# Performance work log

Hardware: AMD Instinct MI355X
Metric: run time of the kernel (lower is better)

Reference implementation:

```python
import jax, jax.numpy as jnp
import numpy as np

B, S = 128, 512
VOCAB, E, H, T = 100000, 100, 128, 10  # tagset_size=10 -> CRF over T-1=9 tags
HD = H // 2  # per-direction LSTM hidden


def setup_inputs():
    key = jax.random.key(0)
    ks = jax.random.split(key, 14)
    s = 0.08
    inputs = jax.random.randint(ks[0], (B, S), 1, VOCAB)
    tags = jax.random.randint(ks[1], (B, S), 1, T)  # valid after tags-1 shift
    mask = jnp.ones((B, S), dtype=bool)
    emb = (jax.random.normal(ks[2], (VOCAB, E)) * s).at[0].set(0.0)  # padding_idx=0 row zeroed
    Wih_f = jax.random.normal(ks[3], (4 * HD, E)) * s
    Whh_f = jax.random.normal(ks[4], (4 * HD, HD)) * s
    b_f = jax.random.normal(ks[5], (4 * HD,)) * s
    Wih_b = jax.random.normal(ks[6], (4 * HD, E)) * s
    Whh_b = jax.random.normal(ks[7], (4 * HD, HD)) * s
    b_b = jax.random.normal(ks[8], (4 * HD,)) * s
    W_out = jax.random.normal(ks[9], (T, H)) * s
    b_out = jax.random.normal(ks[10], (T,)) * s
    start = jax.random.normal(ks[11], (T - 1,)) * s
    end = jax.random.normal(ks[12], (T - 1,)) * s
    trans = jax.random.normal(ks[13], (T - 1, T - 1)) * s
    return dict(inputs=inputs, tags=tags, mask=mask, emb=emb,
                Wih_f=Wih_f, Whh_f=Whh_f, b_f=b_f,
                Wih_b=Wih_b, Whh_b=Whh_b, b_b=b_b,
                W_out=W_out, b_out=b_out, start=start, end=end, trans=trans)


def _lstm_dir(x, Wih, Whh, b, reverse):
    # x: [S, B, E] time-major; PyTorch gate order i,f,g,o; b = b_ih + b_hh
    h0 = jnp.zeros((x.shape[1], Whh.shape[1]), x.dtype)

    def step(carry, xt):
        h, c = carry
        gates = xt @ Wih.T + h @ Whh.T + b
        i, f, g, o = jnp.split(gates, 4, axis=-1)
        c = jax.nn.sigmoid(f) * c + jax.nn.sigmoid(i) * jnp.tanh(g)
        h = jax.nn.sigmoid(o) * jnp.tanh(c)
        return (h, c), h

    _, hs = jax.lax.scan(step, (h0, h0), x, reverse=reverse)
    return hs  # [S, B, HD]


def _crf_nll(em, tags, mask, start, end, trans):
    # Linear-chain CRF (torchcrf-style). em: [S,B,K], tags/mask: [S,B]
    pick = lambda e, t: jnp.take_along_axis(e, t[:, None], axis=-1)[:, 0]
    # numerator: score of the gold path
    score0 = start[tags[0]] + pick(em[0], tags[0])

    def num_step(sc, inp):
        em_t, t, tp, m = inp
        return sc + jnp.where(m, trans[tp, t] + pick(em_t, t), 0.0), None

    score, _ = jax.lax.scan(num_step, score0, (em[1:], tags[1:], tags[:-1], mask[1:]))
    last_idx = mask.sum(0).astype(jnp.int32) - 1
    last_tags = jnp.take_along_axis(tags, last_idx[None, :], axis=0)[0]
    score = score + end[last_tags]
    # denominator: forward algorithm (log partition)
    alpha0 = start[None, :] + em[0]  # [B,K]

    def fwd_step(alpha, inp):
        em_t, m = inp
        nxt = jax.nn.logsumexp(alpha[:, :, None] + trans[None, :, :] + em_t[:, None, :], axis=1)
        return jnp.where(m[:, None], nxt, alpha), None

    alpha, _ = jax.lax.scan(fwd_step, alpha0, (em[1:], mask[1:]))
    logZ = jax.nn.logsumexp(alpha + end[None, :], axis=1)
    return -(score - logZ).mean()  # loss = -log_likelihood.mean()


def _forward(inputs, tags, mask, emb, Wih_f, Whh_f, b_f, Wih_b, Whh_b, b_b, W_out, b_out, start, end, trans):
    x = emb[inputs].transpose(1, 0, 2)  # [S,B,E]
    h = jnp.concatenate([_lstm_dir(x, Wih_f, Whh_f, b_f, False),
                         _lstm_dir(x, Wih_b, Whh_b, b_b, True)], axis=-1)  # [S,B,H]
    # dropout is identity at eval; slice off tag 0 as in the module
    em = (h @ W_out.T + b_out)[:, :, 1:]  # [S,B,T-1]
    return _crf_nll(em, (tags - 1).T, mask.T, start, end, trans)


def reference(inputs, tags, mask, emb, Wih_f, Whh_f, b_f, Wih_b, Whh_b, b_b, W_out, b_out, start, end, trans):
    return _forward(inputs, tags, mask, emb, Wih_f, Whh_f, b_f, Wih_b, Whh_b, b_b, W_out, b_out, start, end, trans)
```

## Files before the change

kernel.cpp:

```cpp
#include <hip/hip_runtime.h>
#include <math.h>

#define SB 512
#define NB 128
#define HD 64

typedef _Float16 h2 __attribute__((ext_vector_type(2)));
union U4 { uint4 u; h2 h[4]; _Float16 f[8]; };
union U2 { uint2 u; _Float16 f[4]; };
union UH { unsigned u; _Float16 f[2]; };

__device__ __forceinline__ float frcp(float x) { return __builtin_amdgcn_rcpf(x); }
__device__ __forceinline__ float fsig(float x) { return frcp(1.0f + __expf(-x)); }
__device__ __forceinline__ float ftanh(float x) {
    float t = __expf(-2.0f * fabsf(x));
    float r = (1.0f - t) * frcp(1.0f + t);
    return copysignf(r, x);
}
__device__ __forceinline__ float fdot2(h2 a, h2 b, float c) {
    return __builtin_amdgcn_fdot2(a, b, c, false);
}

__global__ void prep_kernel(const float* __restrict__ Wih_f, const float* __restrict__ Wih_bb,
                            const float* __restrict__ Whh_f, const float* __restrict__ Whh_bb,
                            const float* __restrict__ b_f, const float* __restrict__ b_bb,
                            const float* __restrict__ trans,
                            unsigned* __restrict__ W2h, unsigned* __restrict__ whh16,
                            float* __restrict__ bias2, float* __restrict__ Eexp)
{
    int idx = blockIdx.x * 256 + threadIdx.x;
    if (idx < 26624) {
        int col = idx / 52, d = idx - col * 52;
        int dir = col >> 8, r = col & 255, j = r >> 2, g = r & 3;
        const float* src = (dir ? Wih_bb : Wih_f) + (g * 64 + j) * 100;
        UH u; u.u = 0;
        if (d < 50) { u.f[0] = (_Float16)src[2 * d]; u.f[1] = (_Float16)src[2 * d + 1]; }
        W2h[idx] = u.u;
    } else if (idx < 43008) {
        int d = idx - 26624;
        int kp = d & 31, u = (d >> 5) & 63, g = (d >> 11) & 3, dir = d >> 13;
        const float* src = (dir ? Whh_bb : Whh_f) + (g * 64 + u) * 64 + 2 * kp;
        UH uu; uu.f[0] = (_Float16)src[0]; uu.f[1] = (_Float16)src[1];
        whh16[d] = uu.u;
    } else if (idx < 43520) {
        int col = idx - 43008;
        int dir = col >> 8, r = col & 255, j = r >> 2, g = r & 3;
        bias2[col] = (dir ? b_bb : b_f)[g * 64 + j];
    } else if (idx < 43601) {
        int i = idx - 43520;
        Eexp[i] = __expf(trans[i]);
    }
}

__global__ __launch_bounds__(256, 1) void gemm_kernel(
    const int* __restrict__ inputs, const float* __restrict__ emb,
    const unsigned* __restrict__ W2h, const float* __restrict__ bias2,
    _Float16* __restrict__ xgh)
{
    __shared__ __align__(16) unsigned sE[128 * 52];
    __shared__ __align__(16) unsigned sW[128 * 52];
    __shared__ int stok[128];
    const int tt = blockIdx.x;
    const int tid = threadIdx.x;

    if (tid < 128) stok[tid] = inputs[tid * SB + tt];
    __syncthreads();
    for (int idx = tid; idx < 6656; idx += 256) {
        int row = idx / 52, d = idx - row * 52;
        int token = stok[row];
        UH u; u.u = 0;
        if (d < 50) {
            const float* ep = emb + (size_t)token * 100 + 2 * d;
            u.f[0] = (_Float16)ep[0]; u.f[1] = (_Float16)ep[1];
        }
        sE[idx] = u.u;
    }

    const int tx = tid & 15, ty = tid >> 4;

    for (int cb4 = 0; cb4 < 4; ++cb4) {
        const int cb = cb4 * 128;
        __syncthreads();
        for (int idx = tid; idx < 1664; idx += 256)
            ((uint4*)sW)[idx] = ((const uint4*)W2h)[cb * 13 + idx];
        __syncthreads();

        float acc[8][8];
        #pragma unroll
        for (int r = 0; r < 8; ++r)
            #pragma unroll
            for (int i = 0; i < 8; ++i) acc[r][i] = 0.f;

        for (int kk = 0; kk < 13; ++kk) {
            U4 e[8], wv[8];
            #pragma unroll
            for (int r = 0; r < 8; ++r) e[r].u = ((const uint4*)sE)[(ty + 16 * r) * 13 + kk];
            #pragma unroll
            for (int i = 0; i < 8; ++i) wv[i].u = ((const uint4*)sW)[(tx + 16 * i) * 13 + kk];
            #pragma unroll
            for (int r = 0; r < 8; ++r)
                #pragma unroll
                for (int i = 0; i < 8; ++i) {
                    float a = acc[r][i];
                    #pragma unroll
                    for (int q = 0; q < 4; ++q) a = fdot2(e[r].h[q], wv[i].h[q], a);
                    acc[r][i] = a;
                }
        }

        #pragma unroll
        for (int i = 0; i < 8; ++i) {
            int col = cb + tx + 16 * i;
            float bc = bias2[col];
            #pragma unroll
            for (int r = 0; r < 8; ++r) {
                int row = tt * NB + ty + 16 * r;
                xgh[(size_t)row * 512 + col] = (_Float16)(acc[r][i] + bc);
            }
        }
    }
}

__global__ __attribute__((amdgpu_flat_work_group_size(64, 64), amdgpu_waves_per_eu(1, 1)))
void lstm_kernel(
    const _Float16* __restrict__ xgh, const unsigned* __restrict__ whh16,
    _Float16* __restrict__ h16)
{
    const int blk = blockIdx.x;
    const int b = blk & (NB - 1);
    const int dir = blk >> 7;
    const int j = threadIdx.x;

    U4 w[32];
    const uint4* W4 = (const uint4*)(whh16 + dir * 8192);
    #pragma unroll
    for (int g = 0; g < 4; ++g)
        #pragma unroll
        for (int k4 = 0; k4 < 8; ++k4)
            w[g * 8 + k4].u = W4[(g * 64 + j) * 8 + k4];
    #pragma unroll
    for (int i = 0; i < 32; ++i)
        asm volatile("" : "+v"(w[i].u.x), "+v"(w[i].u.y), "+v"(w[i].u.z), "+v"(w[i].u.w));

    __shared__ __align__(16) _Float16 hbuf[64];
    hbuf[j] = (_Float16)0.f;
    float c = 0.f;

    const int t0 = dir ? (SB - 1) : 0;
    const ptrdiff_t xstride = (dir ? -1 : 1) * (ptrdiff_t)(NB * 512);
    const _Float16* xp = xgh + ((size_t)(t0 * NB + b)) * 512 + dir * 256 + j * 4;
    _Float16* hp = h16 + ((size_t)(b * 2 + dir) * SB + t0) * 64 + j;
    const ptrdiff_t hstride = (dir ? -1 : 1) * (ptrdiff_t)64;

    U2 p0, p1, p2;
    p0.u = *(const uint2*)xp;
    p1.u = *(const uint2*)(xp + xstride);
    p2.u = *(const uint2*)(xp + 2 * xstride);
    const _Float16* xq = xp + 3 * xstride;

    for (int s = 0; s < SB; ++s) {
        float a0 = (float)p0.f[0], a1 = (float)p0.f[1];
        float a2 = (float)p0.f[2], a3 = (float)p0.f[3];
        p0 = p1; p1 = p2;
        p2.u = *(const uint2*)xq;
        xq += xstride;

        U4 hv[8];
        #pragma unroll
        for (int k4 = 0; k4 < 8; ++k4) hv[k4].u = *(const uint4*)&hbuf[k4 * 8];

        float g0[4] = {a0, 0.f, 0.f, 0.f};
        float g1[4] = {a1, 0.f, 0.f, 0.f};
        float g2[4] = {a2, 0.f, 0.f, 0.f};
        float g3[4] = {a3, 0.f, 0.f, 0.f};
        #pragma unroll
        for (int k4 = 0; k4 < 8; ++k4) {
            const int p = k4 & 3;
            #pragma unroll
            for (int q = 0; q < 4; ++q) {
                g0[p] = fdot2(hv[k4].h[q], w[0 * 8 + k4].h[q], g0[p]);
                g1[p] = fdot2(hv[k4].h[q], w[1 * 8 + k4].h[q], g1[p]);
                g2[p] = fdot2(hv[k4].h[q], w[2 * 8 + k4].h[q], g2[p]);
                g3[p] = fdot2(hv[k4].h[q], w[3 * 8 + k4].h[q], g3[p]);
            }
        }
        a0 = (g0[0] + g0[1]) + (g0[2] + g0[3]);
        a1 = (g1[0] + g1[1]) + (g1[2] + g1[3]);
        a2 = (g2[0] + g2[1]) + (g2[2] + g2[3]);
        a3 = (g3[0] + g3[1]) + (g3[2] + g3[3]);

        float ig = fsig(a0), fg = fsig(a1), gg = ftanh(a2), og = fsig(a3);
        c = fg * c + ig * gg;
        float h = og * ftanh(c);
        *hp = (_Float16)h;
        hp += hstride;
        hbuf[j] = (_Float16)h;
    }
}

__global__ __launch_bounds__(256, 1) void proj_kernel(
    const _Float16* __restrict__ h16, const float* __restrict__ W_out,
    const float* __restrict__ b_out, float* __restrict__ em3)
{
    __shared__ __align__(16) unsigned tile[128 * 64];
    __shared__ __align__(16) unsigned sWo[9 * 64];
    __shared__ float sb[9];
    const int b = blockIdx.x, tid = threadIdx.x;

    for (int i2 = tid; i2 < 576; i2 += 256) {
        int k = i2 >> 6, jp = i2 & 63;
        const float* src = W_out + (k + 1) * 128 + 2 * jp;
        UH u; u.f[0] = (_Float16)src[0]; u.f[1] = (_Float16)src[1];
        sWo[i2] = u.u;
    }
    if (tid < 9) sb[tid] = b_out[1 + tid];

    float* dst0 = em3 + (size_t)b * (SB * 12);

    for (int tt = 0; tt < 4; ++tt) {
        const int t0 = tt * 128;
        __syncthreads();
        #pragma unroll
        for (int dir = 0; dir < 2; ++dir) {
            const unsigned* src = (const unsigned*)(h16 + ((size_t)(b * 2 + dir) * SB + t0) * 64);
            for (int i = tid; i < 4096; i += 256) {
                int t = i >> 5, jp = i & 31;
                tile[t * 64 + dir * 32 + jp] = src[i];
            }
        }
        __syncthreads();

        for (int o = tid; o < 1152; o += 256) {
            int tl = o / 9, k = o - 9 * tl;
            const U4* hr = (const U4*)&tile[tl * 64];
            const U4* wr = (const U4*)&sWo[k * 64];
            float pa = 0.f, pb = 0.f;
            #pragma unroll
            for (int q = 0; q < 16; q += 2) {
                U4 hv = hr[q], wv = wr[q];
                U4 hv2 = hr[q + 1], wv2 = wr[q + 1];
                #pragma unroll
                for (int z = 0; z < 4; ++z) {
                    pa = fdot2(hv.h[z], wv.h[z], pa);
                    pb = fdot2(hv2.h[z], wv2.h[z], pb);
                }
            }
            dst0[(t0 + tl) * 12 + k] = pa + pb + sb[k];
        }
    }
}

__global__ __launch_bounds__(64, 1) void crf_gold(
    const float* __restrict__ em3, const int* __restrict__ tags,
    const float* __restrict__ startv, const float* __restrict__ endv,
    const float* __restrict__ trans, float* __restrict__ gold)
{
    const int b = blockIdx.x, l = threadIdx.x;
    const int* tb = tags + (size_t)b * SB;
    const float* eb = em3 + (size_t)b * (SB * 12);
    float sc = 0.f;
    for (int t = l; t < SB; t += 64) {
        int tg = tb[t] - 1;
        if (t > 0) {
            int tp = tb[t - 1] - 1;
            sc += trans[tp * 9 + tg] + eb[t * 12 + tg];
        }
    }
    if (l == 0) {
        int tg0 = tb[0] - 1, tgl = tb[SB - 1] - 1;
        sc += startv[tg0] + eb[tg0] + endv[tgl];
    }
    #pragma unroll
    for (int off = 32; off > 0; off >>= 1) sc += __shfl_down(sc, off);
    if (l == 0) gold[b] = sc;
}

__global__ __launch_bounds__(256, 1) void crf_scan(
    const float* __restrict__ em3, const float* __restrict__ Eexp,
    float* __restrict__ Pws)
{
    const int lane = blockIdx.x * 256 + threadIdx.x;
    const int c = lane & 31, b = lane >> 5;

    float E[81];
    #pragma unroll
    for (int i = 0; i < 81; ++i) E[i] = Eexp[i];

    float P[81];
    #pragma unroll
    for (int i = 0; i < 81; ++i) P[i] = 0.f;
    #pragma unroll
    for (int i = 0; i < 9; ++i) P[i * 9 + i] = 1.f;
    float M = 0.f;

    const int t0 = 1 + 16 * c;
    const int nst = (t0 + 16 <= SB) ? 16 : (SB - t0);
    const float* ep = em3 + (size_t)b * (SB * 12) + t0 * 12;

    for (int s = 0; s < nst; ++s, ep += 12) {
        float4 e0 = *(const float4*)ep;
        float4 e1 = *(const float4*)(ep + 4);
        float e8 = ep[8];
        float ex[9] = { __expf(e0.x), __expf(e0.y), __expf(e0.z), __expf(e0.w),
                        __expf(e1.x), __expf(e1.y), __expf(e1.z), __expf(e1.w),
                        __expf(e8) };
        #pragma unroll
        for (int i = 0; i < 9; ++i) {
            float tmp[9];
            #pragma unroll
            for (int jj = 0; jj < 9; ++jj) tmp[jj] = P[i * 9] * E[jj];
            #pragma unroll
            for (int k = 1; k < 9; ++k)
                #pragma unroll
                for (int jj = 0; jj < 9; ++jj) tmp[jj] += P[i * 9 + k] * E[k * 9 + jj];
            #pragma unroll
            for (int jj = 0; jj < 9; ++jj) P[i * 9 + jj] = tmp[jj] * ex[jj];
        }
        if ((s & 3) == 3) {
            float mx = P[0];
            #pragma unroll
            for (int i = 1; i < 81; ++i) mx = fmaxf(mx, P[i]);
            M += __logf(mx);
            float r = frcp(mx);
            #pragma unroll
            for (int i = 0; i < 81; ++i) P[i] *= r;
        }
    }

    float* dst = Pws + (size_t)lane * 84;
    #pragma unroll
    for (int i = 0; i < 81; ++i) dst[i] = P[i];
    dst[81] = M;
}

__global__ __launch_bounds__(128, 1) void crf_combine(
    const float* __restrict__ em3, const float* __restrict__ Pws,
    const float* __restrict__ gold, const float* __restrict__ startv,
    const float* __restrict__ endv, float* __restrict__ out)
{
    const int b = threadIdx.x;
    float A[9], M = 0.f;
    {
        const float* eb = em3 + (size_t)b * (SB * 12);
        float4 e0 = *(const float4*)eb;
        float4 e1 = *(const float4*)(eb + 4);
        float e[9] = { e0.x, e0.y, e0.z, e0.w, e1.x, e1.y, e1.z, e1.w, eb[8] };
        #pragma unroll
        for (int k = 0; k < 9; ++k) A[k] = __expf(startv[k] + e[k]);
    }

    for (int c = 0; c < 32; ++c) {
        const float4* src = (const float4*)(Pws + ((size_t)b * 32 + c) * 84);
        float buf[84];
        #pragma unroll
        for (int q = 0; q < 21; ++q) {
            float4 v = src[q];
            buf[4 * q] = v.x; buf[4 * q + 1] = v.y; buf[4 * q + 2] = v.z; buf[4 * q + 3] = v.w;
        }
        float tmp[9];
        #pragma unroll
        for (int jj = 0; jj < 9; ++jj) tmp[jj] = A[0] * buf[jj];
        #pragma unroll
        for (int i = 1; i < 9; ++i)
            #pragma unroll
            for (int jj = 0; jj < 9; ++jj) tmp[jj] += A[i] * buf[i * 9 + jj];
        float mx = tmp[0];
        #pragma unroll
        for (int jj = 1; jj < 9; ++jj) mx = fmaxf(mx, tmp[jj]);
        M += __logf(mx) + buf[81];
        float r = frcp(mx);
        #pragma unroll
        for (int jj = 0; jj < 9; ++jj) A[jj] = tmp[jj] * r;
    }

    float Z = 0.f;
    #pragma unroll
    for (int k = 0; k < 9; ++k) Z += A[k] * __expf(endv[k]);
    float part = M + __logf(Z) - gold[b];

    #pragma unroll
    for (int off = 32; off > 0; off >>= 1) part += __shfl_down(part, off);
    __shared__ float sm[2];
    if ((b & 63) == 0) sm[b >> 6] = part;
    __syncthreads();
    if (b == 0) out[0] = (sm[0] + sm[1]) * (1.0f / NB);
}

extern "C" void kernel_launch(void* const* d_in, const int* in_sizes, int n_in,
                              void* d_out, int out_size, void* d_ws, size_t ws_size,
                              hipStream_t stream)
{
    const int*   inputs = (const int*)d_in[0];
    const int*   tags   = (const int*)d_in[1];
    const float* emb    = (const float*)d_in[3];
    const float* Wih_f  = (const float*)d_in[4];
    const float* Whh_f  = (const float*)d_in[5];
    const float* b_f    = (const float*)d_in[6];
    const float* Wih_b  = (const float*)d_in[7];
    const float* Whh_b  = (const float*)d_in[8];
    const float* b_b    = (const float*)d_in[9];
    const float* W_out  = (const float*)d_in[10];
    const float* b_out  = (const float*)d_in[11];
    const float* startv = (const float*)d_in[12];
    const float* endv   = (const float*)d_in[13];
    const float* transv = (const float*)d_in[14];

    char* w = (char*)d_ws;
    float* em3     = (float*)w;     w += (size_t)NB * SB * 12 * 4;
    _Float16* xgh  = (_Float16*)w;  w += (size_t)SB * NB * 512 * 2;
    _Float16* h16  = (_Float16*)w;  w += (size_t)NB * 2 * SB * 64 * 2;
    float* Pws     = (float*)w;     w += (size_t)NB * 32 * 84 * 4;
    float* gold    = (float*)w;     w += NB * 4;
    unsigned* W2h  = (unsigned*)w;  w += 26624 * 4;
    unsigned* whh16= (unsigned*)w;  w += 16384 * 4;
    float* bias2   = (float*)w;     w += 512 * 4;
    float* Eexp    = (float*)w;     w += 81 * 4;

    prep_kernel<<<171, 256, 0, stream>>>(Wih_f, Wih_b, Whh_f, Whh_b, b_f, b_b, transv,
                                         W2h, whh16, bias2, Eexp);
    gemm_kernel<<<SB, 256, 0, stream>>>(inputs, emb, W2h, bias2, xgh);
    lstm_kernel<<<256, 64, 0, stream>>>(xgh, whh16, h16);
    proj_kernel<<<NB, 256, 0, stream>>>(h16, W_out, b_out, em3);
    crf_gold<<<NB, 64, 0, stream>>>(em3, tags, startv, endv, transv, gold);
    crf_scan<<<16, 256, 0, stream>>>(em3, Eexp, Pws);
    crf_combine<<<1, 128, 0, stream>>>(em3, Pws, gold, startv, endv, (float*)d_out);
}
```

Before: 549.6 us.

## Split LSTM hidden-unit dot products across two lanes with double-buffered h

The LSTM recurrence kernel now runs 128 threads per sequence/direction, with each hidden unit's 64-wide dot product split across a lane pair and combined via a shuffle. Each thread keeps half the recurrent weights in registers. The shared hidden-state buffer is double-buffered and a block barrier is added each step, since two waves now cooperate. This halves the serial per-step FMA chain on the latency-bound recurrence, at the cost of a __syncthreads per timestep and a cross-lane shuffle.

```diff
diff --git a/kernel.cpp b/kernel.cpp
--- a/kernel.cpp
+++ b/kernel.cpp
@@ -121,7 +121,7 @@
     }
 }
 
-__global__ __attribute__((amdgpu_flat_work_group_size(64, 64), amdgpu_waves_per_eu(1, 1)))
+__global__ __attribute__((amdgpu_flat_work_group_size(128, 128), amdgpu_waves_per_eu(1, 1)))
 void lstm_kernel(
     const _Float16* __restrict__ xgh, const unsigned* __restrict__ whh16,
     _Float16* __restrict__ h16)
@@ -129,27 +129,27 @@
     const int blk = blockIdx.x;
     const int b = blk & (NB - 1);
     const int dir = blk >> 7;
-    const int j = threadIdx.x;
-
-    U4 w[32];
-    const uint4* W4 = (const uint4*)(whh16 + dir * 8192);
+    const int tid = threadIdx.x;
+    const int wv = tid >> 6, l = tid & 63;
+    const int u = wv * 32 + (l >> 1);
+    const int kh = l & 1;
+
+    U4 w[4][4];
+    const uint4* W4 = (const uint4*)whh16;
     #pragma unroll
     for (int g = 0; g < 4; ++g)
         #pragma unroll
-        for (int k4 = 0; k4 < 8; ++k4)
-            w[g * 8 + k4].u = W4[(g * 64 + j) * 8 + k4];
-    #pragma unroll
-    for (int i = 0; i < 32; ++i)
-        asm volatile("" : "+v"(w[i].u.x), "+v"(w[i].u.y), "+v"(w[i].u.z), "+v"(w[i].u.w));
-
-    __shared__ __align__(16) _Float16 hbuf[64];
-    hbuf[j] = (_Float16)0.f;
+        for (int q = 0; q < 4; ++q)
+            w[g][q].u = W4[((dir * 4 + g) * 64 + u) * 8 + kh * 4 + q];
+
+    __shared__ __align__(16) _Float16 hbuf[2][64];
+    if (tid < 64) hbuf[0][tid] = (_Float16)0.f;
     float c = 0.f;
 
     const int t0 = dir ? (SB - 1) : 0;
     const ptrdiff_t xstride = (dir ? -1 : 1) * (ptrdiff_t)(NB * 512);
-    const _Float16* xp = xgh + ((size_t)(t0 * NB + b)) * 512 + dir * 256 + j * 4;
-    _Float16* hp = h16 + ((size_t)(b * 2 + dir) * SB + t0) * 64 + j;
+    const _Float16* xp = xgh + ((size_t)(t0 * NB + b)) * 512 + dir * 256 + u * 4;
+    _Float16* hp = h16 + ((size_t)(b * 2 + dir) * SB + t0) * 64 + u;
     const ptrdiff_t hstride = (dir ? -1 : 1) * (ptrdiff_t)64;
 
     U2 p0, p1, p2;
@@ -157,44 +157,45 @@
     p1.u = *(const uint2*)(xp + xstride);
     p2.u = *(const uint2*)(xp + 2 * xstride);
     const _Float16* xq = xp + 3 * xstride;
+    __syncthreads();
 
     for (int s = 0; s < SB; ++s) {
-        float a0 = (float)p0.f[0], a1 = (float)p0.f[1];
-        float a2 = (float)p0.f[2], a3 = (float)p0.f[3];
+        const int par = s & 1;
+        U4 hv[4];
+        #pragma unroll
+        for (int q = 0; q < 4; ++q)
+            hv[q].u = *(const uint4*)&hbuf[par][kh * 32 + q * 8];
+
+        float pa[4], pb[4];
+        #pragma unroll
+        for (int g = 0; g < 4; ++g) { pa[g] = 0.f; pb[g] = 0.f; }
+        #pragma unroll
+        for (int q = 0; q < 4; ++q)
+            #pragma unroll
+            for (int g = 0; g < 4; ++g) {
+                pa[g] = fdot2(hv[q].h[0], w[g][q].h[0], pa[g]);
+                pa[g] = fdot2(hv[q].h[1], w[g][q].h[1], pa[g]);
+                pb[g] = fdot2(hv[q].h[2], w[g][q].h[2], pb[g]);
+                pb[g] = fdot2(hv[q].h[3], w[g][q].h[3], pb[g]);
+            }
+
+        float a[4];
+        #pragma unroll
+        for (int g = 0; g < 4; ++g) {
+            float sg = pa[g] + pb[g];
+            a[g] = sg + __shfl_xor(sg, 1, 64) + (float)p0.f[g];
+        }
         p0 = p1; p1 = p2;
         p2.u = *(const uint2*)xq;
         xq += xstride;
 
-        U4 hv[8];
-        #pragma unroll
-        for (int k4 = 0; k4 < 8; ++k4) hv[k4].u = *(const uint4*)&hbuf[k4 * 8];
-
-        float g0[4] = {a0, 0.f, 0.f, 0.f};
-        float g1[4] = {a1, 0.f, 0.f, 0.f};
-        float g2[4] = {a2, 0.f, 0.f, 0.f};
-        float g3[4] = {a3, 0.f, 0.f, 0.f};
-        #pragma unroll
-        for (int k4 = 0; k4 < 8; ++k4) {
-            const int p = k4 & 3;
-            #pragma unroll
-            for (int q = 0; q < 4; ++q) {
-                g0[p] = fdot2(hv[k4].h[q], w[0 * 8 + k4].h[q], g0[p]);
-                g1[p] = fdot2(hv[k4].h[q], w[1 * 8 + k4].h[q], g1[p]);
-                g2[p] = fdot2(hv[k4].h[q], w[2 * 8 + k4].h[q], g2[p]);
-                g3[p] = fdot2(hv[k4].h[q], w[3 * 8 + k4].h[q], g3[p]);
-            }
-        }
-        a0 = (g0[0] + g0[1]) + (g0[2] + g0[3]);
-        a1 = (g1[0] + g1[1]) + (g1[2] + g1[3]);
-        a2 = (g2[0] + g2[1]) + (g2[2] + g2[3]);
-        a3 = (g3[0] + g3[1]) + (g3[2] + g3[3]);
-
-        float ig = fsig(a0), fg = fsig(a1), gg = ftanh(a2), og = fsig(a3);
+        float ig = fsig(a[0]), fg = fsig(a[1]), gg = ftanh(a[2]), og = fsig(a[3]);
         c = fg * c + ig * gg;
         float h = og * ftanh(c);
-        *hp = (_Float16)h;
+        hbuf[par ^ 1][u] = (_Float16)h;
+        if (kh == 0) *hp = (_Float16)h;
         hp += hstride;
-        hbuf[j] = (_Float16)h;
+        __syncthreads();
     }
 }
 
@@ -419,7 +420,7 @@
     prep_kernel<<<171, 256, 0, stream>>>(Wih_f, Wih_b, Whh_f, Whh_b, b_f, b_b, transv,
                                          W2h, whh16, bias2, Eexp);
     gemm_kernel<<<SB, 256, 0, stream>>>(inputs, emb, W2h, bias2, xgh);
-    lstm_kernel<<<256, 64, 0, stream>>>(xgh, whh16, h16);
+    lstm_kernel<<<256, 128, 0, stream>>>(xgh, whh16, h16);
     proj_kernel<<<NB, 256, 0, stream>>>(h16, W_out, b_out, em3);
     crf_gold<<<NB, 64, 0, stream>>>(em3, tags, startv, endv, transv, gold);
     crf_scan<<<16, 256, 0, stream>>>(em3, Eexp, Pws);
```

After: 556.6 us. About the same (+1.3%).

## Fuse projection and CRF stages into one per-sequence kernel using shared memory

Applied to the files above, without the earlier changes.

Merges the output projection, gold-path score, chunked CRF forward scan and chunk combine into a single kernel per batch row. Emissions and chunk transfer matrices stay in shared memory, and the final loss is accumulated with an atomic add into an output zeroed by a memset. This removes three launches and the global round trips for emissions and partial matrices. In exchange the CRF scan now uses only 32 threads per block on 128 blocks, and the LSTM weight register pinning is removed while a barrier is added before its loop.

```diff
diff --git a/kernel.cpp b/kernel.cpp
--- a/kernel.cpp
+++ b/kernel.cpp
@@ -24,9 +24,8 @@
 __global__ void prep_kernel(const float* __restrict__ Wih_f, const float* __restrict__ Wih_bb,
                             const float* __restrict__ Whh_f, const float* __restrict__ Whh_bb,
                             const float* __restrict__ b_f, const float* __restrict__ b_bb,
-                            const float* __restrict__ trans,
                             unsigned* __restrict__ W2h, unsigned* __restrict__ whh16,
-                            float* __restrict__ bias2, float* __restrict__ Eexp)
+                            float* __restrict__ bias2)
 {
     int idx = blockIdx.x * 256 + threadIdx.x;
     if (idx < 26624) {
@@ -46,9 +45,6 @@
         int col = idx - 43008;
         int dir = col >> 8, r = col & 255, j = r >> 2, g = r & 3;
         bias2[col] = (dir ? b_bb : b_f)[g * 64 + j];
-    } else if (idx < 43601) {
-        int i = idx - 43520;
-        Eexp[i] = __expf(trans[i]);
     }
 }
 
@@ -138,9 +134,6 @@
         #pragma unroll
         for (int k4 = 0; k4 < 8; ++k4)
             w[g * 8 + k4].u = W4[(g * 64 + j) * 8 + k4];
-    #pragma unroll
-    for (int i = 0; i < 32; ++i)
-        asm volatile("" : "+v"(w[i].u.x), "+v"(w[i].u.y), "+v"(w[i].u.z), "+v"(w[i].u.w));
 
     __shared__ __align__(16) _Float16 hbuf[64];
     hbuf[j] = (_Float16)0.f;
@@ -157,6 +150,7 @@
     p1.u = *(const uint2*)(xp + xstride);
     p2.u = *(const uint2*)(xp + 2 * xstride);
     const _Float16* xq = xp + 3 * xstride;
+    __syncthreads();
 
     for (int s = 0; s < SB; ++s) {
         float a0 = (float)p0.f[0], a1 = (float)p0.f[1];
@@ -198,14 +192,21 @@
     }
 }
 
-__global__ __launch_bounds__(256, 1) void proj_kernel(
+__global__ __launch_bounds__(256, 1) void fused_crf(
     const _Float16* __restrict__ h16, const float* __restrict__ W_out,
-    const float* __restrict__ b_out, float* __restrict__ em3)
-{
+    const float* __restrict__ b_out, const int* __restrict__ tags,
+    const float* __restrict__ startv, const float* __restrict__ endv,
+    const float* __restrict__ trans, float* __restrict__ out)
+{
+    __shared__ __align__(16) float emc[16 * 32 * 9];
+    __shared__ __align__(16) float em0[12];
     __shared__ __align__(16) unsigned tile[128 * 64];
     __shared__ __align__(16) unsigned sWo[9 * 64];
     __shared__ float sb[9];
+    __shared__ float sgold;
+
     const int b = blockIdx.x, tid = threadIdx.x;
+    float* chout = (float*)tile;
 
     for (int i2 = tid; i2 < 576; i2 += 256) {
         int k = i2 >> 6, jp = i2 & 63;
@@ -215,8 +216,6 @@
     }
     if (tid < 9) sb[tid] = b_out[1 + tid];
 
-    float* dst0 = em3 + (size_t)b * (SB * 12);
-
     for (int tt = 0; tt < 4; ++tt) {
         const int t0 = tt * 128;
         __syncthreads();
@@ -245,145 +244,117 @@
                     pb = fdot2(hv2.h[z], wv2.h[z], pb);
                 }
             }
-            dst0[(t0 + tl) * 12 + k] = pa + pb + sb[k];
-        }
-    }
-}
-
-__global__ __launch_bounds__(64, 1) void crf_gold(
-    const float* __restrict__ em3, const int* __restrict__ tags,
-    const float* __restrict__ startv, const float* __restrict__ endv,
-    const float* __restrict__ trans, float* __restrict__ gold)
-{
-    const int b = blockIdx.x, l = threadIdx.x;
-    const int* tb = tags + (size_t)b * SB;
-    const float* eb = em3 + (size_t)b * (SB * 12);
-    float sc = 0.f;
-    for (int t = l; t < SB; t += 64) {
-        int tg = tb[t] - 1;
-        if (t > 0) {
-            int tp = tb[t - 1] - 1;
-            sc += trans[tp * 9 + tg] + eb[t * 12 + tg];
-        }
-    }
-    if (l == 0) {
-        int tg0 = tb[0] - 1, tgl = tb[SB - 1] - 1;
-        sc += startv[tg0] + eb[tg0] + endv[tgl];
-    }
-    #pragma unroll
-    for (int off = 32; off > 0; off >>= 1) sc += __shfl_down(sc, off);
-    if (l == 0) gold[b] = sc;
-}
-
-__global__ __launch_bounds__(256, 1) void crf_scan(
-    const float* __restrict__ em3, const float* __restrict__ Eexp,
-    float* __restrict__ Pws)
-{
-    const int lane = blockIdx.x * 256 + threadIdx.x;
-    const int c = lane & 31, b = lane >> 5;
-
-    float E[81];
-    #pragma unroll
-    for (int i = 0; i < 81; ++i) E[i] = Eexp[i];
-
-    float P[81];
-    #pragma unroll
-    for (int i = 0; i < 81; ++i) P[i] = 0.f;
-    #pragma unroll
-    for (int i = 0; i < 9; ++i) P[i * 9 + i] = 1.f;
-    float M = 0.f;
-
-    const int t0 = 1 + 16 * c;
-    const int nst = (t0 + 16 <= SB) ? 16 : (SB - t0);
-    const float* ep = em3 + (size_t)b * (SB * 12) + t0 * 12;
-
-    for (int s = 0; s < nst; ++s, ep += 12) {
-        float4 e0 = *(const float4*)ep;
-        float4 e1 = *(const float4*)(ep + 4);
-        float e8 = ep[8];
-        float ex[9] = { __expf(e0.x), __expf(e0.y), __expf(e0.z), __expf(e0.w),
-                        __expf(e1.x), __expf(e1.y), __expf(e1.z), __expf(e1.w),
-                        __expf(e8) };
-        #pragma unroll
-        for (int i = 0; i < 9; ++i) {
+            float v = pa + pb + sb[k];
+            int t = t0 + tl;
+            if (t == 0) em0[k] = v;
+            else        emc[(((t - 1) & 15) * 32 + ((t - 1) >> 4)) * 9 + k] = v;
+        }
+    }
+    __syncthreads();
+
+    if (tid >= 64 && tid < 128) {
+        const int l = tid - 64;
+        const int* tb = tags + (size_t)b * SB;
+        float sc = 0.f;
+        for (int t = l; t < SB; t += 64) {
+            int tg = tb[t] - 1;
+            if (t > 0) {
+                int tp = tb[t - 1] - 1;
+                sc += trans[tp * 9 + tg] + emc[(((t - 1) & 15) * 32 + ((t - 1) >> 4)) * 9 + tg];
+            }
+        }
+        if (l == 0) {
+            int tg0 = tb[0] - 1, tgl = tb[SB - 1] - 1;
+            sc += startv[tg0] + em0[tg0] + endv[tgl];
+        }
+        #pragma unroll
+        for (int off = 32; off > 0; off >>= 1) sc += __shfl_down(sc, off);
+        if (l == 0) sgold = sc;
+    }
+
+    if (tid < 32) {
+        const int c = tid;
+        float E[81];
+        #pragma unroll
+        for (int i = 0; i < 81; ++i) E[i] = __expf(trans[i]);
+
+        float P[81];
+        #pragma unroll
+        for (int i = 0; i < 81; ++i) P[i] = 0.f;
+        #pragma unroll
+        for (int i = 0; i < 9; ++i) P[i * 9 + i] = 1.f;
+        float M = 0.f;
+
+        const int t0c = 1 + 16 * c;
+        const int nst = (t0c + 16 <= SB) ? 16 : (SB - t0c);
+        for (int s = 0; s < nst; ++s) {
+            const float* ep = &emc[(s * 32 + c) * 9];
+            float ex[9];
+            #pragma unroll
+            for (int k = 0; k < 9; ++k) ex[k] = __expf(ep[k]);
+            #pragma unroll
+            for (int i = 0; i < 9; ++i) {
+                float tmp[9];
+                #pragma unroll
+                for (int jj = 0; jj < 9; ++jj) tmp[jj] = P[i * 9] * E[jj];
+                #pragma unroll
+                for (int k = 1; k < 9; ++k)
+                    #pragma unroll
+                    for (int jj = 0; jj < 9; ++jj) tmp[jj] += P[i * 9 + k] * E[k * 9 + jj];
+                #pragma unroll
+                for (int jj = 0; jj < 9; ++jj) P[i * 9 + jj] = tmp[jj] * ex[jj];
+            }
+            if ((s & 3) == 3) {
+                float mx = P[0];
+                #pragma unroll
+                for (int i = 1; i < 81; ++i) mx = fmaxf(mx, P[i]);
+                M += __logf(mx);
+                float r = frcp(mx);
+                #pragma unroll
+                for (int i = 0; i < 81; ++i) P[i] *= r;
+            }
+        }
+        float* dst = &chout[c * 84];
+        #pragma unroll
+        for (int i = 0; i < 81; ++i) dst[i] = P[i];
+        dst[81] = M;
+    }
+    __syncthreads();
+
+    if (tid == 0) {
+        float A[9], M = 0.f;
+        #pragma unroll
+        for (int k = 0; k < 9; ++k) A[k] = __expf(startv[k] + em0[k]);
+
+        for (int c = 0; c < 32; ++c) {
+            const float4* src = (const float4*)&chout[c * 84];
+            float buf[84];
+            #pragma unroll
+            for (int q = 0; q < 21; ++q) {
+                float4 v = src[q];
+                buf[4 * q] = v.x; buf[4 * q + 1] = v.y; buf[4 * q + 2] = v.z; buf[4 * q + 3] = v.w;
+            }
             float tmp[9];
             #pragma unroll
-            for (int jj = 0; jj < 9; ++jj) tmp[jj] = P[i * 9] * E[jj];
-            #pragma unroll
-            for (int k = 1; k < 9; ++k)
-                #pragma unroll
-                for (int jj = 0; jj < 9; ++jj) tmp[jj] += P[i * 9 + k] * E[k * 9 + jj];
-            #pragma unroll
-            for (int jj = 0; jj < 9; ++jj) P[i * 9 + jj] = tmp[jj] * ex[jj];
-        }
-        if ((s & 3) == 3) {
-            float mx = P[0];
-            #pragma unroll
-            for (int i = 1; i < 81; ++i) mx = fmaxf(mx, P[i]);
-            M += __logf(mx);
+            for (int jj = 0; jj < 9; ++jj) tmp[jj] = A[0] * buf[jj];
+            #pragma unroll
+            for (int i = 1; i < 9; ++i)
+                #pragma unroll
+                for (int jj = 0; jj < 9; ++jj) tmp[jj] += A[i] * buf[i * 9 + jj];
+            float mx = tmp[0];
+            #pragma unroll
+            for (int jj = 1; jj < 9; ++jj) mx = fmaxf(mx, tmp[jj]);
+            M += __logf(mx) + buf[81];
             float r = frcp(mx);
             #pragma unroll
-            for (int i = 0; i < 81; ++i) P[i] *= r;
-        }
-    }
-
-    float* dst = Pws + (size_t)lane * 84;
-    #pragma unroll
-    for (int i = 0; i < 81; ++i) dst[i] = P[i];
-    dst[81] = M;
-}
-
-__global__ __launch_bounds__(128, 1) void crf_combine(
-    const float* __restrict__ em3, const float* __restrict__ Pws,
-    const float* __restrict__ gold, const float* __restrict__ startv,
-    const float* __restrict__ endv, float* __restrict__ out)
-{
-    const int b = threadIdx.x;
-    float A[9], M = 0.f;
-    {
-        const float* eb = em3 + (size_t)b * (SB * 12);
-        float4 e0 = *(const float4*)eb;
-        float4 e1 = *(const float4*)(eb + 4);
-        float e[9] = { e0.x, e0.y, e0.z, e0.w, e1.x, e1.y, e1.z, e1.w, eb[8] };
-        #pragma unroll
-        for (int k = 0; k < 9; ++k) A[k] = __expf(startv[k] + e[k]);
-    }
-
-    for (int c = 0; c < 32; ++c) {
-        const float4* src = (const float4*)(Pws + ((size_t)b * 32 + c) * 84);
-        float buf[84];
-        #pragma unroll
-        for (int q = 0; q < 21; ++q) {
-            float4 v = src[q];
-            buf[4 * q] = v.x; buf[4 * q + 1] = v.y; buf[4 * q + 2] = v.z; buf[4 * q + 3] = v.w;
-        }
-        float tmp[9];
-        #pragma unroll
-        for (int jj = 0; jj < 9; ++jj) tmp[jj] = A[0] * buf[jj];
-        #pragma unroll
-        for (int i = 1; i < 9; ++i)
-            #pragma unroll
-            for (int jj = 0; jj < 9; ++jj) tmp[jj] += A[i] * buf[i * 9 + jj];
-        float mx = tmp[0];
-        #pragma unroll
-        for (int jj = 1; jj < 9; ++jj) mx = fmaxf(mx, tmp[jj]);
-        M += __logf(mx) + buf[81];
-        float r = frcp(mx);
-        #pragma unroll
-        for (int jj = 0; jj < 9; ++jj) A[jj] = tmp[jj] * r;
-    }
-
-    float Z = 0.f;
-    #pragma unroll
-    for (int k = 0; k < 9; ++k) Z += A[k] * __expf(endv[k]);
-    float part = M + __logf(Z) - gold[b];
-
-    #pragma unroll
-    for (int off = 32; off > 0; off >>= 1) part += __shfl_down(part, off);
-    __shared__ float sm[2];
-    if ((b & 63) == 0) sm[b >> 6] = part;
-    __syncthreads();
-    if (b == 0) out[0] = (sm[0] + sm[1]) * (1.0f / NB);
+            for (int jj = 0; jj < 9; ++jj) A[jj] = tmp[jj] * r;
+        }
+        float Z = 0.f;
+        #pragma unroll
+        for (int k = 0; k < 9; ++k) Z += A[k] * __expf(endv[k]);
+        float part = M + __logf(Z) - sgold;
+        atomicAdd(out, part * (1.0f / NB));
+    }
 }
 
 extern "C" void kernel_launch(void* const* d_in, const int* in_sizes, int n_in,
@@ -406,22 +377,18 @@
     const float* transv = (const float*)d_in[14];
 
     char* w = (char*)d_ws;
-    float* em3     = (float*)w;     w += (size_t)NB * SB * 12 * 4;
+    w += 4 * 1024 * 1024;
     _Float16* xgh  = (_Float16*)w;  w += (size_t)SB * NB * 512 * 2;
     _Float16* h16  = (_Float16*)w;  w += (size_t)NB * 2 * SB * 64 * 2;
-    float* Pws     = (float*)w;     w += (size_t)NB * 32 * 84 * 4;
-    float* gold    = (float*)w;     w += NB * 4;
     unsigned* W2h  = (unsigned*)w;  w += 26624 * 4;
     unsigned* whh16= (unsigned*)w;  w += 16384 * 4;
     float* bias2   = (float*)w;     w += 512 * 4;
-    float* Eexp    = (float*)w;     w += 81 * 4;
-
-    prep_kernel<<<171, 256, 0, stream>>>(Wih_f, Wih_b, Whh_f, Whh_b, b_f, b_b, transv,
-                                         W2h, whh16, bias2, Eexp);
+
+    hipMemsetAsync(d_out, 0, sizeof(float), stream);
+    prep_kernel<<<171, 256, 0, stream>>>(Wih_f, Wih_b, Whh_f, Whh_b, b_f, b_b,
+                                         W2h, whh16, bias2);
     gemm_kernel<<<SB, 256, 0, stream>>>(inputs, emb, W2h, bias2, xgh);
     lstm_kernel<<<256, 64, 0, stream>>>(xgh, whh16, h16);
-    proj_kernel<<<NB, 256, 0, stream>>>(h16, W_out, b_out, em3);
-    crf_gold<<<NB, 64, 0, stream>>>(em3, tags, startv, endv, transv, gold);
-    crf_scan<<<16, 256, 0, stream>>>(em3, Eexp, Pws);
-    crf_combine<<<1, 128, 0, stream>>>(em3, Pws, gold, startv, endv, (float*)d_out);
-}
+    fused_crf<<<NB, 256, 0, stream>>>(h16, W_out, b_out, tags, startv, endv, transv,
+                                      (float*)d_out);
+}
```

After: 536.2 us. -2.4%, faster.
